# Kernel optimization log

Measured on AMD Instinct MI355X. Metric: run time of the kernel, lower is better.

Reference implementation:

```python
import jax, jax.numpy as jnp
import numpy as np

B, T, IN, H, OUT = 256, 512, 8, 128, 3


def setup_inputs() -> dict:
    key = jax.random.key(0)
    ks = jax.random.split(key, 16)
    s = 1.0 / np.sqrt(H)  # PyTorch LSTM init bound

    def u(k, shape):
        return jax.random.uniform(k, shape, jnp.float32, -s, s)

    inp = {"x": jax.random.normal(ks[0], (B, T, IN), jnp.float32)}
    ins = [IN, H, H]
    i = 1
    for l in range(3):
        inp[f"Wih{l}"] = u(ks[i], (4 * H, ins[l]))
        inp[f"Whh{l}"] = u(ks[i + 1], (4 * H, H))
        inp[f"bih{l}"] = u(ks[i + 2], (4 * H,))
        inp[f"bhh{l}"] = u(ks[i + 3], (4 * H,))
        i += 4
    inp["Wfc"] = u(ks[13], (OUT, H))
    inp["bfc"] = u(ks[14], (OUT,))
    return inp


def _lstm_layer(x, Wih, Whh, bih, bhh):
    # x: [T, B, in] -> (all hidden states [T, B, H], final hidden [B, H])
    # Precompute input contribution for every timestep (one big GEMM).
    xg = jnp.einsum('tbi,gi->tbg', x, Wih) + (bih + bhh)  # [T, B, 4H]

    def step(carry, xg_t):
        h, c = carry
        gates = xg_t + h @ Whh.T  # [B, 4H]
        i_, f_, g_, o_ = jnp.split(gates, 4, axis=-1)  # PyTorch gate order i,f,g,o
        c = jax.nn.sigmoid(f_) * c + jax.nn.sigmoid(i_) * jnp.tanh(g_)
        h = jax.nn.sigmoid(o_) * jnp.tanh(c)
        return (h, c), h

    h0 = jnp.zeros((x.shape[1], Whh.shape[1]), x.dtype)
    (hT, _), hs = jax.lax.scan(step, (h0, h0), xg)
    return hs, hT


def reference(x, Wih0, Whh0, bih0, bhh0, Wih1, Whh1, bih1, bhh1,
              Wih2, Whh2, bih2, bhh2, Wfc, bfc):
    xt = jnp.swapaxes(x, 0, 1)  # [T, B, IN]
    h1, _ = _lstm_layer(xt, Wih0, Whh0, bih0, bhh0)
    h2, _ = _lstm_layer(h1, Wih1, Whh1, bih1, bhh1)
    _, hT = _lstm_layer(h2, Wih2, Whh2, bih2, bhh2)  # only last step needed
    return hT @ Wfc.T + bfc  # [B, OUT]
```

## Files before the change

### kernel.cpp

```cpp
#include <hip/hip_runtime.h>

#define Bsz 256
#define Tt  512
#define Hh  128

#define OFF_WTHH 196608
#define OFF_BIAS 393216
#define OFF_HBUF 394752
#define OFF_FLAG 787968
#define FLAG_N   6144

#define SKG(k) ((((k) >> 3) * 12) + ((k) & 7))

__device__ __forceinline__ void st_f32_agent(float* p, float v) {
    __hip_atomic_store(p, v, __ATOMIC_RELAXED, __HIP_MEMORY_SCOPE_AGENT);
}
__device__ __forceinline__ float2 ld_f2_agent(const float* p) {
    unsigned long long u = __hip_atomic_load((unsigned long long*)p,
                                             __ATOMIC_RELAXED, __HIP_MEMORY_SCOPE_AGENT);
    float2 r;
    r.x = __uint_as_float((unsigned int)(u & 0xffffffffull));
    r.y = __uint_as_float((unsigned int)(u >> 32));
    return r;
}

template<int N>
__device__ __forceinline__ float row_shr_add(float v) {
    int s = __builtin_amdgcn_update_dpp(0, __float_as_int(v), 0x110 + N, 0xF, 0xF, true);
    return v + __int_as_float(s);
}
__device__ __forceinline__ float4 red16(float4 s) {
    s.x = row_shr_add<1>(s.x); s.x = row_shr_add<2>(s.x); s.x = row_shr_add<4>(s.x); s.x = row_shr_add<8>(s.x);
    s.y = row_shr_add<1>(s.y); s.y = row_shr_add<2>(s.y); s.y = row_shr_add<4>(s.y); s.y = row_shr_add<8>(s.y);
    s.z = row_shr_add<1>(s.z); s.z = row_shr_add<2>(s.z); s.z = row_shr_add<4>(s.z); s.z = row_shr_add<8>(s.z);
    s.w = row_shr_add<1>(s.w); s.w = row_shr_add<2>(s.w); s.w = row_shr_add<4>(s.w); s.w = row_shr_add<8>(s.w);
    return s;
}

#define FMA4(S, A, W) { S.x = fmaf(A, W.x, S.x); S.y = fmaf(A, W.y, S.y); \
                        S.z = fmaf(A, W.z, S.z); S.w = fmaf(A, W.w, S.w); }

__global__ void prep_kernel(const float* Wih0, const float* Whh0, const float* bih0, const float* bhh0,
                            const float* Wih1, const float* Whh1, const float* bih1, const float* bhh1,
                            const float* Wih2, const float* Whh2, const float* bih2, const float* bhh2,
                            float* ws)
{
    int gid = blockIdx.x * blockDim.x + threadIdx.x;
    for (int i = gid; i < FLAG_N; i += 1536)
        ((int*)(ws + OFF_FLAG))[i] = -1;
    if (gid >= 3 * 512) return;
    int l = gid >> 9, gc = gid & 511;
    const float* Wih = (l == 0) ? Wih0 : (l == 1) ? Wih1 : Wih2;
    const float* Whh = (l == 0) ? Whh0 : (l == 1) ? Whh1 : Whh2;
    const float* bih = (l == 0) ? bih0 : (l == 1) ? bih1 : bih2;
    const float* bhh = (l == 0) ? bhh0 : (l == 1) ? bhh1 : bhh2;
    int Kin = (l == 0) ? 8 : 128;
    float* Wt_ih = ws + (size_t)l * 128 * 512;
    float* Wt_hh = ws + OFF_WTHH + (size_t)l * 128 * 512;
    float* bias  = ws + OFF_BIAS + l * 512;
    for (int k = 0; k < 128; k++) Wt_ih[k * 512 + gc] = (k < Kin) ? Wih[gc * Kin + k] : 0.f;
    for (int k = 0; k < 128; k++) Wt_hh[k * 512 + gc] = Whh[gc * 128 + k];
    bias[gc] = bih[gc] + bhh[gc];
}

__global__ __launch_bounds__(512, 2) void lstm_kernel(const float* __restrict__ x,
                                                      float* __restrict__ ws)
{
    const float* __restrict__ bias = ws + OFF_BIAS;
    float* __restrict__ hbuf = ws + OFF_HBUF;
    int* __restrict__ fl = (int*)(ws + OFF_FLAG);

    const int layer = blockIdx.x >> 6;
    const int tile  = blockIdx.x & 63;
    const int rt  = tile & 15;
    const int hct = tile >> 4;
    const int r0  = rt << 4;
    const int hc0 = hct << 5;
    const int tid = threadIdx.x;

    __shared__ float sAin[16][192];
    __shared__ float sArec[16][192];
    __shared__ float sG[16][132];

    for (int i = tid; i < 16 * 192; i += 512) ((float*)sAin)[i] = 0.f;

    int* myflag = fl + ((layer * 16 + rt) * 4 + hct) * 32;
    int* depp = nullptr;
    int minT = 0;
    int tsub = 1;
    if (tid < 12) {
        int g = tid >> 2, h = tid & 3;
        if (g == 0) {
            depp = fl + ((layer * 16 + rt) * 4 + h) * 32;  minT = 1;  tsub = 1;
        } else if (g == 1) {
            if (layer > 0) { depp = fl + (((layer - 1) * 16 + rt) * 4 + h) * 32; minT = 0; tsub = 1; }
        } else {
            if (layer < 2) { depp = fl + (((layer + 1) * 16 + rt) * 4 + h) * 32; minT = 3 - layer; tsub = 3; }
        }
    }

    const int kg = tid & 15;
    const int rg = (tid >> 4) & 1;
    const int cg = tid >> 5;
    const int cbase = cg << 3;
    const int gcb = ((cbase >> 5) << 7) + hc0 + (cbase & 31);
    const int ka = kg * 12;

    const float* Wl_ih = ws + (size_t)layer * 65536;
    const float* Wl_hh = ws + OFF_WTHH + (size_t)layer * 65536;
    float4 wihA[8], wihB[8], whhA[8], whhB[8];
#pragma unroll
    for (int kk = 0; kk < 8; kk++) {
        int k = kg * 8 + kk;
        wihA[kk] = *(const float4*)&Wl_ih[(size_t)k * 512 + gcb];
        wihB[kk] = *(const float4*)&Wl_ih[(size_t)k * 512 + gcb + 4];
        whhA[kk] = *(const float4*)&Wl_hh[(size_t)k * 512 + gcb];
        whhB[kk] = *(const float4*)&Wl_hh[(size_t)k * 512 + gcb + 4];
    }
    float4 bias4a = *(const float4*)&bias[layer * 512 + gcb];
    float4 bias4b = *(const float4*)&bias[layer * 512 + gcb + 4];
    if (kg != 15) {
        bias4a = make_float4(0.f, 0.f, 0.f, 0.f);
        bias4b = make_float4(0.f, 0.f, 0.f, 0.f);
    }

    const int sr = tid >> 5;
    const int sk = (tid & 31) << 2;
    const int skc = SKG(sk);

    const int ur = tid >> 5, uc = tid & 31;
    float creg = 0.f;

    __syncthreads();

    for (int t = 0; t < Tt; ++t) {
        const int s = t + layer;
        const int prev = (s - 1) & 3, cur = s & 3;

        if (depp != nullptr && t >= minT) {
            const int target = s - tsub;
            while (__hip_atomic_load(depp, __ATOMIC_RELAXED, __HIP_MEMORY_SCOPE_AGENT) < target)
                ;
        }
        __syncthreads();

        if (layer == 0) {
            if (tid < 128) {
                int r = tid >> 3, i = tid & 7;
                sAin[r][i] = x[((size_t)(r0 + r) * Tt + t) * 8 + i];
            }
        } else {
            const float* src = hbuf + ((size_t)prev * 3 + (layer - 1)) * Bsz * Hh
                             + (size_t)(r0 + sr) * Hh + sk;
            float2 p0 = ld_f2_agent(src);
            float2 p1 = ld_f2_agent(src + 2);
            *(float4*)&sAin[sr][skc] = make_float4(p0.x, p0.y, p1.x, p1.y);
        }
        if (t > 0) {
            const float* src = hbuf + ((size_t)prev * 3 + layer) * Bsz * Hh
                             + (size_t)(r0 + sr) * Hh + sk;
            float2 p0 = ld_f2_agent(src);
            float2 p1 = ld_f2_agent(src + 2);
            *(float4*)&sArec[sr][skc] = make_float4(p0.x, p0.y, p1.x, p1.y);
        }
        __syncthreads();

#pragma unroll
        for (int j = 0; j < 8; j++) {
            const int r = rg * 8 + j;
            float4 acc0 = bias4a, acc1 = bias4b;
            {
                float4 a0 = *(const float4*)&sAin[r][ka];
                float4 a1 = *(const float4*)&sAin[r][ka + 4];
                FMA4(acc0, a0.x, wihA[0]); FMA4(acc1, a0.x, wihB[0]);
                FMA4(acc0, a0.y, wihA[1]); FMA4(acc1, a0.y, wihB[1]);
                FMA4(acc0, a0.z, wihA[2]); FMA4(acc1, a0.z, wihB[2]);
                FMA4(acc0, a0.w, wihA[3]); FMA4(acc1, a0.w, wihB[3]);
                FMA4(acc0, a1.x, wihA[4]); FMA4(acc1, a1.x, wihB[4]);
                FMA4(acc0, a1.y, wihA[5]); FMA4(acc1, a1.y, wihB[5]);
                FMA4(acc0, a1.z, wihA[6]); FMA4(acc1, a1.z, wihB[6]);
                FMA4(acc0, a1.w, wihA[7]); FMA4(acc1, a1.w, wihB[7]);
            }
            if (t > 0) {
                float4 b0 = *(const float4*)&sArec[r][ka];
                float4 b1 = *(const float4*)&sArec[r][ka + 4];
                FMA4(acc0, b0.x, whhA[0]); FMA4(acc1, b0.x, whhB[0]);
                FMA4(acc0, b0.y, whhA[1]); FMA4(acc1, b0.y, whhB[1]);
                FMA4(acc0, b0.z, whhA[2]); FMA4(acc1, b0.z, whhB[2]);
                FMA4(acc0, b0.w, whhA[3]); FMA4(acc1, b0.w, whhB[3]);
                FMA4(acc0, b1.x, whhA[4]); FMA4(acc1, b1.x, whhB[4]);
                FMA4(acc0, b1.y, whhA[5]); FMA4(acc1, b1.y, whhB[5]);
                FMA4(acc0, b1.z, whhA[6]); FMA4(acc1, b1.z, whhB[6]);
                FMA4(acc0, b1.w, whhA[7]); FMA4(acc1, b1.w, whhB[7]);
            }
            acc0 = red16(acc0);
            acc1 = red16(acc1);
            if (kg == 15) {
                *(float4*)&sG[r][cbase]     = acc0;
                *(float4*)&sG[r][cbase + 4] = acc1;
            }
        }
        __syncthreads();

        float* hcur = hbuf + ((size_t)cur * 3 + layer) * Bsz * Hh;
        {
            float gi = sG[ur][uc],      gf = sG[ur][32 + uc];
            float gg = sG[ur][64 + uc], go = sG[ur][96 + uc];
            float si = 1.f / (1.f + __expf(-gi));
            float sf = 1.f / (1.f + __expf(-gf));
            float so = 1.f / (1.f + __expf(-go));
            creg = sf * creg + si * tanhf(gg);
            st_f32_agent(&hcur[(size_t)(r0 + ur) * Hh + hc0 + uc], so * tanhf(creg));
        }
        __syncthreads();

        if (tid == 0)
            __hip_atomic_store(myflag, s, __ATOMIC_RELAXED, __HIP_MEMORY_SCOPE_AGENT);
    }
}

__global__ void fc_kernel(const float* __restrict__ ws, const float* __restrict__ Wfc,
                          const float* __restrict__ bfc, float* __restrict__ out)
{
    const float* h2 = ws + OFF_HBUF + (size_t)(1 * 3 + 2) * Bsz * Hh;
    int b = threadIdx.x;
    float a0 = bfc[0], a1 = bfc[1], a2 = bfc[2];
    for (int k = 0; k < 128; k++) {
        float h = h2[b * 128 + k];
        a0 += h * Wfc[0 * 128 + k];
        a1 += h * Wfc[1 * 128 + k];
        a2 += h * Wfc[2 * 128 + k];
    }
    out[b * 3 + 0] = a0;
    out[b * 3 + 1] = a1;
    out[b * 3 + 2] = a2;
}

extern "C" void kernel_launch(void* const* d_in, const int* in_sizes, int n_in,
                              void* d_out, int out_size, void* d_ws, size_t ws_size,
                              hipStream_t stream)
{
    const float* x = (const float*)d_in[0];
    float* ws = (float*)d_ws;

    prep_kernel<<<6, 256, 0, stream>>>(
        (const float*)d_in[1],  (const float*)d_in[2],  (const float*)d_in[3],  (const float*)d_in[4],
        (const float*)d_in[5],  (const float*)d_in[6],  (const float*)d_in[7],  (const float*)d_in[8],
        (const float*)d_in[9],  (const float*)d_in[10], (const float*)d_in[11], (const float*)d_in[12],
        ws);

    void* args[2] = { (void*)&x, (void*)&ws };
    hipLaunchCooperativeKernel((void*)lstm_kernel, dim3(192), dim3(512), args, 0, stream);

    fc_kernel<<<1, 256, 0, stream>>>(ws, (const float*)d_in[13], (const float*)d_in[14], (float*)d_out);
}
```

Baseline: 3.236 ms.

## Tag hidden-state values with sequence numbers to replace flag-based producer waits

Each hidden-state element is now stored as a 64-bit word that packs the float with its timestep sequence number. Consumers spin on the data itself until the tags match, so they no longer wait on per-tile flags before reading. The only flag left is a consumption flag that guards buffer reuse within the 4-slot ring, and it is published right after staging instead of after the store. This removes a block barrier and a flag round-trip per step, but doubles the traffic and footprint of the hidden-state buffer and requires the prep kernel to initialise it.

New measurement: 3.223 ms, median of 4. No clear change (-0.4%).

```diff
diff --git a/kernel.cpp b/kernel.cpp
--- a/kernel.cpp
+++ b/kernel.cpp
@@ -7,21 +7,34 @@
 #define OFF_WTHH 196608
 #define OFF_BIAS 393216
 #define OFF_HBUF 394752
-#define OFF_FLAG 787968
+#define OFF_FLAG 1181184
 #define FLAG_N   6144
 
 #define SKG(k) ((((k) >> 3) * 12) + ((k) & 7))
 
-__device__ __forceinline__ void st_f32_agent(float* p, float v) {
-    __hip_atomic_store(p, v, __ATOMIC_RELAXED, __HIP_MEMORY_SCOPE_AGENT);
-}
-__device__ __forceinline__ float2 ld_f2_agent(const float* p) {
-    unsigned long long u = __hip_atomic_load((unsigned long long*)p,
-                                             __ATOMIC_RELAXED, __HIP_MEMORY_SCOPE_AGENT);
-    float2 r;
-    r.x = __uint_as_float((unsigned int)(u & 0xffffffffull));
-    r.y = __uint_as_float((unsigned int)(u >> 32));
-    return r;
+typedef unsigned long long u64;
+typedef unsigned int u32;
+
+__device__ __forceinline__ void st_h_agent(u64* p, float v, u32 seq) {
+    u64 u = ((u64)seq << 32) | (u64)__float_as_uint(v);
+    __hip_atomic_store(p, u, __ATOMIC_RELAXED, __HIP_MEMORY_SCOPE_AGENT);
+}
+__device__ __forceinline__ u64 ld_u64_agent(const u64* p) {
+    return __hip_atomic_load(p, __ATOMIC_RELAXED, __HIP_MEMORY_SCOPE_AGENT);
+}
+
+__device__ __forceinline__ float4 stage4(const u64* __restrict__ src, u32 exp) {
+    u64 a, b, c, d;
+    for (;;) {
+        a = ld_u64_agent(src + 0);
+        b = ld_u64_agent(src + 1);
+        c = ld_u64_agent(src + 2);
+        d = ld_u64_agent(src + 3);
+        if ((u32)(a >> 32) == exp && (u32)(b >> 32) == exp &&
+            (u32)(c >> 32) == exp && (u32)(d >> 32) == exp) break;
+    }
+    return make_float4(__uint_as_float((u32)a), __uint_as_float((u32)b),
+                       __uint_as_float((u32)c), __uint_as_float((u32)d));
 }
 
 template<int N>
@@ -46,8 +59,9 @@
                             float* ws)
 {
     int gid = blockIdx.x * blockDim.x + threadIdx.x;
-    for (int i = gid; i < FLAG_N; i += 1536)
-        ((int*)(ws + OFF_FLAG))[i] = -1;
+    if (gid < FLAG_N) ((int*)(ws + OFF_FLAG))[gid] = -1;
+    u64* hb = (u64*)(ws + OFF_HBUF);
+    for (int i = gid; i < 4 * 3 * 256 * 128; i += 6144) hb[i] = 0xFFFFFFFF00000000ull;
     if (gid >= 3 * 512) return;
     int l = gid >> 9, gc = gid & 511;
     const float* Wih = (l == 0) ? Wih0 : (l == 1) ? Wih1 : Wih2;
@@ -67,7 +81,7 @@
                                                       float* __restrict__ ws)
 {
     const float* __restrict__ bias = ws + OFF_BIAS;
-    float* __restrict__ hbuf = ws + OFF_HBUF;
+    u64* __restrict__ hbuf = (u64*)(ws + OFF_HBUF);
     int* __restrict__ fl = (int*)(ws + OFF_FLAG);
 
     const int layer = blockIdx.x >> 6;
@@ -84,20 +98,10 @@
 
     for (int i = tid; i < 16 * 192; i += 512) ((float*)sAin)[i] = 0.f;
 
+    int* adflag = nullptr;
+    if (tid < 4)                    adflag = fl + ((layer * 16 + rt) * 4 + tid) * 32;
+    else if (tid < 8 && layer < 2)  adflag = fl + (((layer + 1) * 16 + rt) * 4 + (tid - 4)) * 32;
     int* myflag = fl + ((layer * 16 + rt) * 4 + hct) * 32;
-    int* depp = nullptr;
-    int minT = 0;
-    int tsub = 1;
-    if (tid < 12) {
-        int g = tid >> 2, h = tid & 3;
-        if (g == 0) {
-            depp = fl + ((layer * 16 + rt) * 4 + h) * 32;  minT = 1;  tsub = 1;
-        } else if (g == 1) {
-            if (layer > 0) { depp = fl + (((layer - 1) * 16 + rt) * 4 + h) * 32; minT = 0; tsub = 1; }
-        } else {
-            if (layer < 2) { depp = fl + (((layer + 1) * 16 + rt) * 4 + h) * 32; minT = 3 - layer; tsub = 3; }
-        }
-    }
 
     const int kg = tid & 15;
     const int rg = (tid >> 4) & 1;
@@ -136,13 +140,13 @@
     for (int t = 0; t < Tt; ++t) {
         const int s = t + layer;
         const int prev = (s - 1) & 3, cur = s & 3;
-
-        if (depp != nullptr && t >= minT) {
-            const int target = s - tsub;
-            while (__hip_atomic_load(depp, __ATOMIC_RELAXED, __HIP_MEMORY_SCOPE_AGENT) < target)
+        const u32 expseq = (u32)(s - 1);
+
+        if (adflag != nullptr) {
+            const int target = s - 3;
+            while (__hip_atomic_load(adflag, __ATOMIC_RELAXED, __HIP_MEMORY_SCOPE_AGENT) < target)
                 ;
         }
-        __syncthreads();
 
         if (layer == 0) {
             if (tid < 128) {
@@ -150,20 +154,19 @@
                 sAin[r][i] = x[((size_t)(r0 + r) * Tt + t) * 8 + i];
             }
         } else {
-            const float* src = hbuf + ((size_t)prev * 3 + (layer - 1)) * Bsz * Hh
-                             + (size_t)(r0 + sr) * Hh + sk;
-            float2 p0 = ld_f2_agent(src);
-            float2 p1 = ld_f2_agent(src + 2);
-            *(float4*)&sAin[sr][skc] = make_float4(p0.x, p0.y, p1.x, p1.y);
+            const u64* src = hbuf + ((size_t)prev * 3 + (layer - 1)) * Bsz * Hh
+                           + (size_t)(r0 + sr) * Hh + sk;
+            *(float4*)&sAin[sr][skc] = stage4(src, expseq);
         }
         if (t > 0) {
-            const float* src = hbuf + ((size_t)prev * 3 + layer) * Bsz * Hh
-                             + (size_t)(r0 + sr) * Hh + sk;
-            float2 p0 = ld_f2_agent(src);
-            float2 p1 = ld_f2_agent(src + 2);
-            *(float4*)&sArec[sr][skc] = make_float4(p0.x, p0.y, p1.x, p1.y);
+            const u64* src = hbuf + ((size_t)prev * 3 + layer) * Bsz * Hh
+                           + (size_t)(r0 + sr) * Hh + sk;
+            *(float4*)&sArec[sr][skc] = stage4(src, expseq);
         }
         __syncthreads();
+
+        if (tid == 0)
+            __hip_atomic_store(myflag, s, __ATOMIC_RELAXED, __HIP_MEMORY_SCOPE_AGENT);
 
 #pragma unroll
         for (int j = 0; j < 8; j++) {
@@ -202,7 +205,6 @@
         }
         __syncthreads();
 
-        float* hcur = hbuf + ((size_t)cur * 3 + layer) * Bsz * Hh;
         {
             float gi = sG[ur][uc],      gf = sG[ur][32 + uc];
             float gg = sG[ur][64 + uc], go = sG[ur][96 + uc];
@@ -210,23 +212,21 @@
             float sf = 1.f / (1.f + __expf(-gf));
             float so = 1.f / (1.f + __expf(-go));
             creg = sf * creg + si * tanhf(gg);
-            st_f32_agent(&hcur[(size_t)(r0 + ur) * Hh + hc0 + uc], so * tanhf(creg));
-        }
-        __syncthreads();
-
-        if (tid == 0)
-            __hip_atomic_store(myflag, s, __ATOMIC_RELAXED, __HIP_MEMORY_SCOPE_AGENT);
+            u64* dst = hbuf + ((size_t)cur * 3 + layer) * Bsz * Hh
+                     + (size_t)(r0 + ur) * Hh + hc0 + uc;
+            st_h_agent(dst, so * tanhf(creg), (u32)s);
+        }
     }
 }
 
 __global__ void fc_kernel(const float* __restrict__ ws, const float* __restrict__ Wfc,
                           const float* __restrict__ bfc, float* __restrict__ out)
 {
-    const float* h2 = ws + OFF_HBUF + (size_t)(1 * 3 + 2) * Bsz * Hh;
+    const u64* h2 = (const u64*)(ws + OFF_HBUF) + (size_t)(1 * 3 + 2) * Bsz * Hh;
     int b = threadIdx.x;
     float a0 = bfc[0], a1 = bfc[1], a2 = bfc[2];
     for (int k = 0; k < 128; k++) {
-        float h = h2[b * 128 + k];
+        float h = __uint_as_float((u32)h2[b * 128 + k]);
         a0 += h * Wfc[0 * 128 + k];
         a1 += h * Wfc[1 * 128 + k];
         a2 += h * Wfc[2 * 128 + k];
@@ -243,7 +243,7 @@
     const float* x = (const float*)d_in[0];
     float* ws = (float*)d_ws;
 
-    prep_kernel<<<6, 256, 0, stream>>>(
+    prep_kernel<<<24, 256, 0, stream>>>(
         (const float*)d_in[1],  (const float*)d_in[2],  (const float*)d_in[3],  (const float*)d_in[4],
         (const float*)d_in[5],  (const float*)d_in[6],  (const float*)d_in[7],  (const float*)d_in[8],
         (const float*)d_in[9],  (const float*)d_in[10], (const float*)d_in[11], (const float*)d_in[12],
```
